# Optimization experiments

Measured on AMD Instinct MI355X. Metric: run time of the kernel, lower is better.

The kernel has to match this reference:

```python
import jax, jax.numpy as jnp
import numpy as np

FT_SIZE = 512
NUM_BUCKETS = 8
HID = 32
IN_FEATS = 770

def _crelu(x):
    return jnp.clip(x, 0.0, 1.0)

def setup_inputs() -> dict:
    key = jax.random.key(0)
    ks = jax.random.split(key, 8)
    B = 65536
    x = jax.random.uniform(ks[0], (B, 2 * IN_FEATS), dtype=jnp.float32)
    s = 0.05
    ft_w = jax.random.normal(ks[1], (FT_SIZE, IN_FEATS), dtype=jnp.float32) * s
    ft_b = jax.random.normal(ks[2], (FT_SIZE,), dtype=jnp.float32) * s
    h1_w = jax.random.normal(ks[3], (NUM_BUCKETS, HID, 2 * FT_SIZE), dtype=jnp.float32) * s
    h1_b = jax.random.normal(ks[4], (NUM_BUCKETS, HID), dtype=jnp.float32) * s
    h2_w = jax.random.normal(ks[5], (NUM_BUCKETS, HID, HID), dtype=jnp.float32) * s
    h2_b = jax.random.normal(ks[6], (NUM_BUCKETS, HID), dtype=jnp.float32) * s
    h3_w = jax.random.normal(ks[7], (NUM_BUCKETS, 1, HID), dtype=jnp.float32) * s
    h3_b = jnp.zeros((NUM_BUCKETS, 1), dtype=jnp.float32)
    return {"x": x, "ft_w": ft_w, "ft_b": ft_b, "h1_w": h1_w, "h1_b": h1_b,
            "h2_w": h2_w, "h2_b": h2_b, "h3_w": h3_w, "h3_b": h3_b}

def reference(x, ft_w, ft_b, h1_w, h1_b, h2_w, h2_b, h3_w, h3_b):
    stm = x[:, :IN_FEATS]          # [B, 770]
    nstm = x[:, IN_FEATS:]         # [B, 770]
    stm_ft = _crelu(stm @ ft_w.T + ft_b)    # [B, FT]
    nstm_ft = _crelu(nstm @ ft_w.T + ft_b)  # [B, FT]
    combined = jnp.concatenate([stm_ft, nstm_ft], axis=1)  # [B, 2FT]
    # bucket index from piece count (STM first 768 channels)
    pc = jnp.sum(x[:, :768], axis=1)
    bucket_idx = jnp.clip((pc * NUM_BUCKETS / 33.0).astype(jnp.int32), 0, NUM_BUCKETS - 1)  # [B]
    # compute all bucket heads (dense compute-all, matching original loop+stack)
    h = _crelu(jnp.einsum('bi,koi->bko', combined, h1_w) + h1_b)  # [B, K, 32]
    h = _crelu(jnp.einsum('bko,kpo->bkp', h, h2_w) + h2_b)        # [B, K, 32]
    all_out = jnp.einsum('bko,kpo->bkp', h, h3_w) + h3_b          # [B, K, 1]
    out = jnp.take_along_axis(all_out, bucket_idx[:, None, None], axis=1)  # [B,1,1]
    return out[:, 0, :]  # [B, 1]
```

## Files before the change

kernel.cpp:

```cpp
#include <hip/hip_runtime.h>
#include <hip/hip_bf16.h>
#include <stdint.h>


#define INF  770
#define XROW 1540
#define KP   800
#define FT   512
#define K2   1024
#define N2   256

typedef _Float16 half8 __attribute__((ext_vector_type(8)));
typedef float floatx4 __attribute__((ext_vector_type(4)));
typedef float floatx2 __attribute__((ext_vector_type(2)));

__device__ __forceinline__ float crelu_f(float v) {
    return v < 0.f ? 0.f : (v > 1.f ? 1.f : v);
}

__device__ __forceinline__ void gl_lds16(const _Float16* g, _Float16* l) {
    __builtin_amdgcn_global_load_lds(
        (__attribute__((address_space(1))) void*)(uintptr_t)(const void*)g,
        (__attribute__((address_space(3))) void*)l,
        16, 0, 0);
}

__global__ __launch_bounds__(256) void convert_w_kernel(
    const float* __restrict__ ftw, const float* __restrict__ h1w,
    _Float16* __restrict__ ftw16, _Float16* __restrict__ h1w16)
{
    int idx = blockIdx.x * 256 + threadIdx.x;
    const int FTW = FT * KP;
    if (idx < FTW) {
        int r = idx / KP, c = idx - r * KP;
        ftw16[idx] = (_Float16)(c < INF ? ftw[r * INF + c] : 0.f);
    } else {
        int j = idx - FTW;
        if (j < N2 * K2) h1w16[j] = (_Float16)h1w[j];
    }
}

__global__ __launch_bounds__(512, 4) void gemm_ft_fused(
    const float* __restrict__ x,
    const _Float16* __restrict__ Bt,
    const float* __restrict__ bias,
    _Float16* __restrict__ C,
    int* __restrict__ bucket, int B)
{
    __shared__ _Float16 lsA[128 * 32];
    __shared__ _Float16 lsB[256 * 32];
    int bid = blockIdx.x;
    int xcd = bid & 7, g = bid >> 3;
    int nt = g & 1, mt = (g >> 1) * 8 + xcd;
    int m0 = mt * 128, n0 = nt * 256;
    int tid = threadIdx.x, lane = tid & 63, w = tid >> 6;
    int rm = (w & 1) * 64, rn = (w >> 1) * 64;
    int colL = lane & 15, rowQ = lane >> 4;
    int chA = rowQ ^ ((colL >> 1) & 3);

    int arow = tid >> 2, kq = tid & 3;
    const float* asrc = (m0 < B)
        ? x + (size_t)(m0 + arow) * XROW
        : x + (size_t)(m0 - B + arow) * XROW + INF;
    _Float16* adst = lsA + arow * 32 + (kq ^ ((arow >> 1) & 3)) * 8;

    floatx4 acc[4][4] = {};
    float psum = 0.f;

    for (int kt = 0; kt < 25; ++kt) {
        int ks = kt * 32;
        half8 hv = {};
        if (kt < 24) {
            const float* p = asrc + ks + kq * 8;
            floatx2 f0 = *(const floatx2*)(p);
            floatx2 f1 = *(const floatx2*)(p + 2);
            floatx2 f2 = *(const floatx2*)(p + 4);
            floatx2 f3 = *(const floatx2*)(p + 6);
            hv[0] = (_Float16)f0.x; hv[1] = (_Float16)f0.y;
            hv[2] = (_Float16)f1.x; hv[3] = (_Float16)f1.y;
            hv[4] = (_Float16)f2.x; hv[5] = (_Float16)f2.y;
            hv[6] = (_Float16)f3.x; hv[7] = (_Float16)f3.y;
            psum += (f0.x + f0.y) + (f1.x + f1.y) + (f2.x + f2.y) + (f3.x + f3.y);
        } else if (kq == 0) {
            floatx2 f0 = *(const floatx2*)(asrc + 768);
            hv[0] = (_Float16)f0.x; hv[1] = (_Float16)f0.y;
        }
        *(half8*)adst = hv;
        #pragma unroll
        for (int p = 0; p < 2; ++p) {
            int idx = p * 512 + tid;
            int br = idx >> 2, bs = (idx & 3) ^ ((br >> 1) & 3);
            gl_lds16(Bt + (size_t)(n0 + br) * KP + ks + bs * 8, lsB + idx * 8);
        }
        asm volatile("s_waitcnt vmcnt(0)" ::: "memory");
        __syncthreads();

        half8 af[4], bf[4];
        #pragma unroll
        for (int i = 0; i < 4; ++i)
            af[i] = *(const half8*)(lsA + (rm + i * 16 + colL) * 32 + chA * 8);
        #pragma unroll
        for (int j = 0; j < 4; ++j)
            bf[j] = *(const half8*)(lsB + (rn + j * 16 + colL) * 32 + chA * 8);
        #pragma unroll
        for (int i = 0; i < 4; ++i)
            #pragma unroll
            for (int j = 0; j < 4; ++j)
                acc[i][j] = __builtin_amdgcn_mfma_f32_16x16x32_f16(af[i], bf[j], acc[i][j], 0, 0, 0);
        __syncthreads();
    }

    psum += __shfl_xor(psum, 1, 64);
    psum += __shfl_xor(psum, 2, 64);
    if (nt == 0 && m0 < B && (tid & 3) == 0) {
        int bk = (int)(psum * (8.0f / 33.0f));
        bucket[m0 + arow] = bk < 0 ? 0 : (bk > 7 ? 7 : bk);
    }

    #pragma unroll
    for (int j = 0; j < 4; ++j) {
        int gn = n0 + rn + j * 16 + colL;
        float bv = bias[gn];
        #pragma unroll
        for (int i = 0; i < 4; ++i) {
            #pragma unroll
            for (int r = 0; r < 4; ++r) {
                int gm = m0 + rm + i * 16 + rowQ * 4 + r;
                C[(size_t)gm * FT + gn] = (_Float16)crelu_f(acc[i][j][r] + bv);
            }
        }
    }
}

__global__ __launch_bounds__(512, 4) void gemm_h1_kernel(
    const _Float16* __restrict__ C1,
    const _Float16* __restrict__ Bt,
    const float* __restrict__ bias,
    float* __restrict__ H,
    int B)
{
    __shared__ _Float16 lsA[64 * 32];
    __shared__ _Float16 lsB[256 * 32];
    int m0 = blockIdx.x * 64;
    int tid = threadIdx.x, lane = tid & 63, w = tid >> 6;
    int colL = lane & 15, rowQ = lane >> 4;
    int chA = rowQ ^ ((colL >> 1) & 3);

    floatx4 acc[4][2] = {};

    for (int kt = 0; kt < 32; ++kt) {
        int ks = kt * 32;
        const _Float16* Abase = (ks < FT) ? (C1 + (size_t)m0 * FT + ks)
                                          : (C1 + (size_t)(B + m0) * FT + (ks - FT));
        if (tid < 256) {
            int br = tid >> 2, bs = (tid & 3) ^ ((br >> 1) & 3);
            gl_lds16(Abase + (size_t)br * FT + bs * 8, lsA + tid * 8);
        }
        #pragma unroll
        for (int p = 0; p < 2; ++p) {
            int idx = p * 512 + tid;
            int br = idx >> 2, bs = (idx & 3) ^ ((br >> 1) & 3);
            gl_lds16(Bt + (size_t)br * K2 + ks + bs * 8, lsB + idx * 8);
        }
        asm volatile("s_waitcnt vmcnt(0)" ::: "memory");
        __syncthreads();

        half8 af[4], bf[2];
        #pragma unroll
        for (int i = 0; i < 4; ++i)
            af[i] = *(const half8*)(lsA + (i * 16 + colL) * 32 + chA * 8);
        #pragma unroll
        for (int j = 0; j < 2; ++j)
            bf[j] = *(const half8*)(lsB + (w * 32 + j * 16 + colL) * 32 + chA * 8);
        #pragma unroll
        for (int i = 0; i < 4; ++i)
            #pragma unroll
            for (int j = 0; j < 2; ++j)
                acc[i][j] = __builtin_amdgcn_mfma_f32_16x16x32_f16(af[i], bf[j], acc[i][j], 0, 0, 0);
        __syncthreads();
    }

    #pragma unroll
    for (int j = 0; j < 2; ++j) {
        int gn = w * 32 + j * 16 + colL;
        float bv = bias[gn];
        #pragma unroll
        for (int i = 0; i < 4; ++i) {
            #pragma unroll
            for (int r = 0; r < 4; ++r) {
                int gm = m0 + i * 16 + rowQ * 4 + r;
                H[(size_t)gm * N2 + gn] = crelu_f(acc[i][j][r] + bv);
            }
        }
    }
}

__global__ __launch_bounds__(256) void tail_kernel(
    const float* __restrict__ H,
    const int* __restrict__ bucket,
    const float* __restrict__ h2w,
    const float* __restrict__ h2b,
    const float* __restrict__ h3w,
    const float* __restrict__ h3b,
    float* __restrict__ out, int B)
{
    int s = blockIdx.x * 8 + (threadIdx.x >> 5);
    int j = threadIdx.x & 31;
    if (s >= B) return;
    int k = bucket[s];
    float h1v = H[(size_t)s * N2 + k * 32 + j];
    const float* w2 = h2w + ((k * 32 + j) * 32);
    float a = h2b[k * 32 + j];
    #pragma unroll
    for (int i = 0; i < 32; ++i) a += w2[i] * __shfl(h1v, i, 32);
    a = crelu_f(a);
    float p = a * h3w[k * 32 + j];
    #pragma unroll
    for (int off = 16; off; off >>= 1) p += __shfl_down(p, off, 32);
    if (j == 0) out[s] = p + h3b[k];
}

extern "C" void kernel_launch(void* const* d_in, const int* in_sizes, int n_in,
                              void* d_out, int out_size, void* d_ws, size_t ws_size,
                              hipStream_t stream) {
    const float* x    = (const float*)d_in[0];
    const float* ftw  = (const float*)d_in[1];
    const float* ftb  = (const float*)d_in[2];
    const float* h1w  = (const float*)d_in[3];
    const float* h1b  = (const float*)d_in[4];
    const float* h2w  = (const float*)d_in[5];
    const float* h2b  = (const float*)d_in[6];
    const float* h3w  = (const float*)d_in[7];
    const float* h3b  = (const float*)d_in[8];
    float* out = (float*)d_out;

    int B = in_sizes[0] / (2 * INF);

    char* ws = (char*)d_ws;
    _Float16* C1    = (_Float16*)ws;
    size_t c1_b     = (size_t)2 * B * FT * sizeof(_Float16);
    _Float16* ftw16 = (_Float16*)(ws + c1_b);
    size_t ftw_b    = (size_t)FT * KP * sizeof(_Float16);
    _Float16* h1w16 = (_Float16*)(ws + c1_b + ftw_b);
    size_t h1w_b    = (size_t)N2 * K2 * sizeof(_Float16);
    int* bucket     = (int*)(ws + c1_b + ftw_b + h1w_b);
    size_t bk_b     = (size_t)B * sizeof(int);
    float* H        = (float*)(ws + c1_b + ftw_b + h1w_b + bk_b);

    {
        int total = FT * KP + N2 * K2;
        convert_w_kernel<<<(total + 255) / 256, 256, 0, stream>>>(ftw, h1w, ftw16, h1w16);
    }
    gemm_ft_fused<<<(2 * B / 128) * 2, 512, 0, stream>>>(x, ftw16, ftb, C1, bucket, B);
    gemm_h1_kernel<<<B / 64, 512, 0, stream>>>(C1, h1w16, h1b, H, B);
    tail_kernel<<<(B + 7) / 8, 256, 0, stream>>>(H, bucket, h2w, h2b, h3w, h3b, out, B);
}
```

Before: 799.4 us.

## Double-buffer LDS tiles in both GEMM kernels to overlap loads with MFMA

Both the feature-transformer GEMM and the hidden-layer-1 GEMM now keep two LDS tile buffers. The next k-tile's global-to-LDS copies, and the fp32 x loads now widened to 16 bytes, are issued before the MFMAs on the current tile, leaving one barrier per iteration. This is meant to hide global-memory latency behind matrix math. It doubles LDS per block (48 KB in the FT kernel), which may lower occupancy. It also drops the explicit vmcnt wait and relies on the barrier to order the async LDS writes.

```diff
diff --git a/kernel.cpp b/kernel.cpp
--- a/kernel.cpp
+++ b/kernel.cpp
@@ -47,8 +47,8 @@
     _Float16* __restrict__ C,
     int* __restrict__ bucket, int B)
 {
-    __shared__ _Float16 lsA[128 * 32];
-    __shared__ _Float16 lsB[256 * 32];
+    __shared__ _Float16 lsA[2][128 * 32];
+    __shared__ _Float16 lsB[2][256 * 32];
     int bid = blockIdx.x;
     int xcd = bid & 7, g = bid >> 3;
     int nt = g & 1, mt = (g >> 1) * 8 + xcd;
@@ -62,51 +62,77 @@
     const float* asrc = (m0 < B)
         ? x + (size_t)(m0 + arow) * XROW
         : x + (size_t)(m0 - B + arow) * XROW + INF;
-    _Float16* adst = lsA + arow * 32 + (kq ^ ((arow >> 1) & 3)) * 8;
+    int adoff = arow * 32 + (kq ^ ((arow >> 1) & 3)) * 8;
+
+    floatx2 edge;
+    if (kq == 0) edge = *(const floatx2*)(asrc + 768);
 
     floatx4 acc[4][4] = {};
     float psum = 0.f;
 
+    {
+        const float* p = asrc + kq * 8;
+        floatx4 f01 = *(const floatx4*)p;
+        floatx4 f23 = *(const floatx4*)(p + 4);
+        half8 hv;
+        hv[0] = (_Float16)f01.x; hv[1] = (_Float16)f01.y;
+        hv[2] = (_Float16)f01.z; hv[3] = (_Float16)f01.w;
+        hv[4] = (_Float16)f23.x; hv[5] = (_Float16)f23.y;
+        hv[6] = (_Float16)f23.z; hv[7] = (_Float16)f23.w;
+        psum += (f01.x + f01.y) + (f01.z + f01.w) + (f23.x + f23.y) + (f23.z + f23.w);
+        *(half8*)(lsA[0] + adoff) = hv;
+        #pragma unroll
+        for (int p2 = 0; p2 < 2; ++p2) {
+            int idx = p2 * 512 + tid;
+            int br = idx >> 2, bs = (idx & 3) ^ ((br >> 1) & 3);
+            gl_lds16(Bt + (size_t)(n0 + br) * KP + bs * 8, lsB[0] + idx * 8);
+        }
+    }
+    __syncthreads();
+
     for (int kt = 0; kt < 25; ++kt) {
-        int ks = kt * 32;
-        half8 hv = {};
-        if (kt < 24) {
-            const float* p = asrc + ks + kq * 8;
-            floatx2 f0 = *(const floatx2*)(p);
-            floatx2 f1 = *(const floatx2*)(p + 2);
-            floatx2 f2 = *(const floatx2*)(p + 4);
-            floatx2 f3 = *(const floatx2*)(p + 6);
-            hv[0] = (_Float16)f0.x; hv[1] = (_Float16)f0.y;
-            hv[2] = (_Float16)f1.x; hv[3] = (_Float16)f1.y;
-            hv[4] = (_Float16)f2.x; hv[5] = (_Float16)f2.y;
-            hv[6] = (_Float16)f3.x; hv[7] = (_Float16)f3.y;
-            psum += (f0.x + f0.y) + (f1.x + f1.y) + (f2.x + f2.y) + (f3.x + f3.y);
-        } else if (kq == 0) {
-            floatx2 f0 = *(const floatx2*)(asrc + 768);
-            hv[0] = (_Float16)f0.x; hv[1] = (_Float16)f0.y;
-        }
-        *(half8*)adst = hv;
-        #pragma unroll
-        for (int p = 0; p < 2; ++p) {
-            int idx = p * 512 + tid;
-            int br = idx >> 2, bs = (idx & 3) ^ ((br >> 1) & 3);
-            gl_lds16(Bt + (size_t)(n0 + br) * KP + ks + bs * 8, lsB + idx * 8);
-        }
-        asm volatile("s_waitcnt vmcnt(0)" ::: "memory");
-        __syncthreads();
-
+        int cur = kt & 1, nxt = cur ^ 1;
+        bool full = (kt + 1 < 24);
+        floatx4 f01, f23;
+        if (full) {
+            const float* p = asrc + (kt + 1) * 32 + kq * 8;
+            f01 = *(const floatx4*)p;
+            f23 = *(const floatx4*)(p + 4);
+        }
+        if (kt + 1 < 25) {
+            int ks = (kt + 1) * 32;
+            #pragma unroll
+            for (int p2 = 0; p2 < 2; ++p2) {
+                int idx = p2 * 512 + tid;
+                int br = idx >> 2, bs = (idx & 3) ^ ((br >> 1) & 3);
+                gl_lds16(Bt + (size_t)(n0 + br) * KP + ks + bs * 8, lsB[nxt] + idx * 8);
+            }
+        }
         half8 af[4], bf[4];
         #pragma unroll
         for (int i = 0; i < 4; ++i)
-            af[i] = *(const half8*)(lsA + (rm + i * 16 + colL) * 32 + chA * 8);
+            af[i] = *(const half8*)(lsA[cur] + (rm + i * 16 + colL) * 32 + chA * 8);
         #pragma unroll
         for (int j = 0; j < 4; ++j)
-            bf[j] = *(const half8*)(lsB + (rn + j * 16 + colL) * 32 + chA * 8);
+            bf[j] = *(const half8*)(lsB[cur] + (rn + j * 16 + colL) * 32 + chA * 8);
         #pragma unroll
         for (int i = 0; i < 4; ++i)
             #pragma unroll
             for (int j = 0; j < 4; ++j)
                 acc[i][j] = __builtin_amdgcn_mfma_f32_16x16x32_f16(af[i], bf[j], acc[i][j], 0, 0, 0);
+        if (kt + 1 < 25) {
+            half8 hv = {};
+            if (full) {
+                hv[0] = (_Float16)f01.x; hv[1] = (_Float16)f01.y;
+                hv[2] = (_Float16)f01.z; hv[3] = (_Float16)f01.w;
+                hv[4] = (_Float16)f23.x; hv[5] = (_Float16)f23.y;
+                hv[6] = (_Float16)f23.z; hv[7] = (_Float16)f23.w;
+                psum += (f01.x + f01.y) + (f01.z + f01.w) + (f23.x + f23.y) + (f23.z + f23.w);
+            } else if (kq == 0) {
+                hv[0] = (_Float16)edge.x; hv[1] = (_Float16)edge.y;
+            }
+            *(half8*)(lsA[nxt] + adoff) = hv;
+        }
         __syncthreads();
     }
 
@@ -139,8 +165,8 @@
     float* __restrict__ H,
     int B)
 {
-    __shared__ _Float16 lsA[64 * 32];
-    __shared__ _Float16 lsB[256 * 32];
+    __shared__ _Float16 lsA[2][64 * 32];
+    __shared__ _Float16 lsB[2][256 * 32];
     int m0 = blockIdx.x * 64;
     int tid = threadIdx.x, lane = tid & 63, w = tid >> 6;
     int colL = lane & 15, rowQ = lane >> 4;
@@ -148,30 +174,36 @@
 
     floatx4 acc[4][2] = {};
 
+    #define H1_STAGE(KT, BUF) do {                                              \
+        int ks_ = (KT) * 32;                                                    \
+        const _Float16* Abase_ = (ks_ < FT)                                     \
+            ? (C1 + (size_t)m0 * FT + ks_)                                      \
+            : (C1 + (size_t)(B + m0) * FT + (ks_ - FT));                        \
+        if (tid < 256) {                                                        \
+            int br_ = tid >> 2, bs_ = (tid & 3) ^ ((br_ >> 1) & 3);             \
+            gl_lds16(Abase_ + (size_t)br_ * FT + bs_ * 8, lsA[BUF] + tid * 8);  \
+        }                                                                       \
+        _Pragma("unroll")                                                       \
+        for (int p2_ = 0; p2_ < 2; ++p2_) {                                     \
+            int idx_ = p2_ * 512 + tid;                                         \
+            int br_ = idx_ >> 2, bs_ = (idx_ & 3) ^ ((br_ >> 1) & 3);           \
+            gl_lds16(Bt + (size_t)br_ * K2 + ks_ + bs_ * 8, lsB[BUF] + idx_ * 8); \
+        }                                                                       \
+    } while (0)
+
+    H1_STAGE(0, 0);
+    __syncthreads();
+
     for (int kt = 0; kt < 32; ++kt) {
-        int ks = kt * 32;
-        const _Float16* Abase = (ks < FT) ? (C1 + (size_t)m0 * FT + ks)
-                                          : (C1 + (size_t)(B + m0) * FT + (ks - FT));
-        if (tid < 256) {
-            int br = tid >> 2, bs = (tid & 3) ^ ((br >> 1) & 3);
-            gl_lds16(Abase + (size_t)br * FT + bs * 8, lsA + tid * 8);
-        }
-        #pragma unroll
-        for (int p = 0; p < 2; ++p) {
-            int idx = p * 512 + tid;
-            int br = idx >> 2, bs = (idx & 3) ^ ((br >> 1) & 3);
-            gl_lds16(Bt + (size_t)br * K2 + ks + bs * 8, lsB + idx * 8);
-        }
-        asm volatile("s_waitcnt vmcnt(0)" ::: "memory");
-        __syncthreads();
-
+        int cur = kt & 1, nxt = cur ^ 1;
+        if (kt + 1 < 32) H1_STAGE(kt + 1, nxt);
         half8 af[4], bf[2];
         #pragma unroll
         for (int i = 0; i < 4; ++i)
-            af[i] = *(const half8*)(lsA + (i * 16 + colL) * 32 + chA * 8);
+            af[i] = *(const half8*)(lsA[cur] + (i * 16 + colL) * 32 + chA * 8);
         #pragma unroll
         for (int j = 0; j < 2; ++j)
-            bf[j] = *(const half8*)(lsB + (w * 32 + j * 16 + colL) * 32 + chA * 8);
+            bf[j] = *(const half8*)(lsB[cur] + (w * 32 + j * 16 + colL) * 32 + chA * 8);
         #pragma unroll
         for (int i = 0; i < 4; ++i)
             #pragma unroll
@@ -179,6 +211,7 @@
                 acc[i][j] = __builtin_amdgcn_mfma_f32_16x16x32_f16(af[i], bf[j], acc[i][j], 0, 0, 0);
         __syncthreads();
     }
+    #undef H1_STAGE
 
     #pragma unroll
     for (int j = 0; j < 2; ++j) {
```

Measured after the change: 829.4 us. +3.8%, slower.
